# Kernel tuning notes

Hardware: AMD Instinct MI355X
Metric: run time of the kernel (lower is better)

The kernel has to match this reference:

```python
import jax, jax.numpy as jnp
import numpy as np

ALPHA = 0.2
EPS = 0.05        # geomloss SamplesLoss(p=1, blur=0.05): eps = blur**p = 0.05
N_ITERS = 50      # fixed sinkhorn iteration budget


def _sqdist(x, y):
    # x: [N,3], y: [M,3] -> [N,M] squared euclidean distances
    d2 = (jnp.sum(x * x, 1)[:, None] + jnp.sum(y * y, 1)[None, :]
          - 2.0 * (x @ y.T))
    return jnp.maximum(d2, 0.0)


def _sinkhorn_value(C, eps, n_iters):
    # uniform weights, log-domain sinkhorn; returns dual OT value <a,f>+<b,g>
    N, M = C.shape
    loga = -jnp.log(jnp.float32(N))
    logb = -jnp.log(jnp.float32(M))

    def step(carry, _):
        f, g = carry
        f = -eps * jax.nn.logsumexp(logb + (g[None, :] - C) / eps, axis=1)
        g = -eps * jax.nn.logsumexp(loga + (f[:, None] - C) / eps, axis=0)
        return (f, g), None

    (f, g), _ = jax.lax.scan(step, (jnp.zeros(N, C.dtype), jnp.zeros(M, C.dtype)),
                             None, length=n_iters)
    return jnp.mean(f) + jnp.mean(g)


def _sinkhorn_divergence(x, y, eps, n_iters):
    # debiased sinkhorn divergence: OT(x,y) - 0.5 OT(x,x) - 0.5 OT(y,y)
    def cost(a, b):
        return jnp.sqrt(_sqdist(a, b) + 1e-12)  # p=1 cost ||x-y||
    ot_xy = _sinkhorn_value(cost(x, y), eps, n_iters)
    ot_xx = _sinkhorn_value(cost(x, x), eps, n_iters)
    ot_yy = _sinkhorn_value(cost(y, y), eps, n_iters)
    return ot_xy - 0.5 * ot_xx - 0.5 * ot_yy


def setup_inputs() -> dict:
    key = jax.random.key(0)
    k1, k2 = jax.random.split(key)
    pred_feat = jax.random.normal(k1, (8192, 4), dtype=jnp.float32)
    gt_feat = jax.random.normal(k2, (8192, 4), dtype=jnp.float32)
    return {"pred_feat": pred_feat, "gt_feat": gt_feat}


def reference(pred_feat, gt_feat):
    pred_xyz = pred_feat[:, :3]
    gt_xyz = gt_feat[:, :3]
    # one-directional chamfer gt -> pred, squared NN distance, mean reduction
    d2 = _sqdist(gt_xyz, pred_xyz)          # [Ngt, Npred]
    chamfer_loss = jnp.mean(jnp.min(d2, axis=1))
    emd_loss = _sinkhorn_divergence(pred_xyz, gt_xyz, EPS, N_ITERS)
    return ALPHA * chamfer_loss + (1.0 - ALPHA) * emd_loss
```

## Files before the change

### kernel.cpp

```cpp
#include <hip/hip_runtime.h>
#include <hip/hip_bf16.h>
#include <math.h>


#define PN 8192
#define EPS 0.05f
#define SCALE 28.853900817779268f
#define INV_S2 (1.0f / (SCALE * SCALE))
#define LN2 0.6931471805599453f
#define TILE 2048
#define MARGIN 14.0f

#define EXP2F __builtin_amdgcn_exp2f
#define SQRTF __builtin_amdgcn_sqrtf
#if defined(__has_builtin) && __has_builtin(__builtin_amdgcn_logf)
#define LOG2F __builtin_amdgcn_logf
#else
#define LOG2F log2f
#endif

__device__ __forceinline__ int bitrev8(int x) { return __brev(x) >> 24; }

#define WS_QP    0
#define WS_QG    131072
#define WS_VF    262144
#define WS_VG    360448
#define WS_BB32  458752
#define WS_BB64  475136
#define WS_SARR  483328
#define WS_CHAM  532480

__global__ __launch_bounds__(1024) void sort_kernel(
    const float4* __restrict__ pred, const float4* __restrict__ gt,
    float4* __restrict__ QP, float4* __restrict__ QG)
{
    const int cloud = blockIdx.x;
    const float4* src = cloud ? gt : pred;
    float4* dst = cloud ? QG : QP;
    const int tid = threadIdx.x;

    __shared__ int hist[4096];
    __shared__ int part[1024];
#pragma unroll
    for (int k = 0; k < 4; ++k) hist[tid * 4 + k] = 0;
    __syncthreads();

    int keys[8];
#pragma unroll
    for (int k = 0; k < 8; ++k) {
        float4 v = src[tid * 8 + k];
        int cx = min(15, max(0, (int)floorf((v.x + 5.0f) * 1.6f)));
        int cy = min(15, max(0, (int)floorf((v.y + 5.0f) * 1.6f)));
        int cz = min(15, max(0, (int)floorf((v.z + 5.0f) * 1.6f)));
        keys[k] = (cz << 8) | (cy << 4) | cx;
        atomicAdd(&hist[keys[k]], 1);
    }
    __syncthreads();
    int h[4], s4 = 0;
#pragma unroll
    for (int k = 0; k < 4; ++k) { h[k] = hist[tid * 4 + k]; s4 += h[k]; }
    part[tid] = s4;
    __syncthreads();
    for (int off = 1; off < 1024; off <<= 1) {
        int v = (tid >= off) ? part[tid - off] : 0;
        __syncthreads();
        part[tid] += v;
        __syncthreads();
    }
    int base = part[tid] - s4;
#pragma unroll
    for (int k = 0; k < 4; ++k) { hist[tid * 4 + k] = base; base += h[k]; }
    __syncthreads();
#pragma unroll
    for (int k = 0; k < 8; ++k) {
        float4 v = src[tid * 8 + k];
        int pos = atomicAdd(&hist[keys[k]], 1);
        float x = v.x * SCALE, y = v.y * SCALE, z = v.z * SCALE;
        dst[pos] = make_float4(x, y, z, fmaf(x, x, fmaf(y, y, z * z)));
    }
}

__global__ __launch_bounds__(64) void bbox32_kernel(
    const float4* __restrict__ QP, const float4* __restrict__ QG,
    float4* __restrict__ bb32)
{
    const int b = blockIdx.x;
    const float4* q = (b >> 8) ? QG : QP;
    const int lane = threadIdx.x;
    float4 v = q[(b & 255) * 32 + (lane & 31)];
    float lx = v.x, ly = v.y, lz = v.z, hx = v.x, hy = v.y, hz = v.z;
#pragma unroll
    for (int off = 1; off <= 16; off <<= 1) {
        lx = fminf(lx, __shfl_xor(lx, off, 64));
        ly = fminf(ly, __shfl_xor(ly, off, 64));
        lz = fminf(lz, __shfl_xor(lz, off, 64));
        hx = fmaxf(hx, __shfl_xor(hx, off, 64));
        hy = fmaxf(hy, __shfl_xor(hy, off, 64));
        hz = fmaxf(hz, __shfl_xor(hz, off, 64));
    }
    if (lane == 0) {
        bb32[b * 2]     = make_float4(lx, ly, lz, 0.0f);
        bb32[b * 2 + 1] = make_float4(hx, hy, hz, 0.0f);
    }
}

__global__ __launch_bounds__(256) void bbox64_kernel(
    const float4* __restrict__ bb32, float4* __restrict__ bb64)
{
    const int t = threadIdx.x;
    const int cloud = t >> 7, tile = t & 127;
    const int s = (cloud * 256 + tile * 2) * 2;
    float4 lo0 = bb32[s], hi0 = bb32[s + 1], lo1 = bb32[s + 2], hi1 = bb32[s + 3];
    bb64[t * 2] = make_float4(fminf(lo0.x, lo1.x), fminf(lo0.y, lo1.y),
                              fminf(lo0.z, lo1.z), 0.0f);
    bb64[t * 2 + 1] = make_float4(fmaxf(hi0.x, hi1.x), fmaxf(hi0.y, hi1.y),
                                  fmaxf(hi0.z, hi1.z), 0.0f);
}

__global__ __launch_bounds__(256) void init_kernel(
    float* __restrict__ Vg, float* __restrict__ chamsum)
{
    int idx = blockIdx.x * 256 + threadIdx.x;
    if (idx < 3 * PN) Vg[idx] = 1.0f / 8192.0f;
    if (idx == 0) *chamsum = 0.0f;
}

__global__ __launch_bounds__(256) void seed_kernel(
    const float4* __restrict__ QP, const float4* __restrict__ QG,
    const float4* __restrict__ bb32, float* __restrict__ SArr)
{
    const int idx = blockIdx.x * 256 + threadIdx.x;
    const int quarter = idx & 3;
    const int rg = (idx >> 2) & 2047;
    const int combo = idx >> 13;
    const float4* rowQ = (combo >= 2) ? QG : QP;
    const int colCloud = (combo == 0 || combo == 2) ? 1 : 0;

    float lx = 1e30f, ly = 1e30f, lz = 1e30f;
    float hx = -1e30f, hy = -1e30f, hz = -1e30f;
#pragma unroll
    for (int k = 0; k < 4; ++k) {
        float4 q = rowQ[rg * 4 + k];
        lx = fminf(lx, q.x); hx = fmaxf(hx, q.x);
        ly = fminf(ly, q.y); hy = fmaxf(hy, q.y);
        lz = fminf(lz, q.z); hz = fmaxf(hz, q.z);
    }
    float best = 1e30f;
    for (int t = quarter * 64; t < quarter * 64 + 64; ++t) {
        float4 lo = bb32[(colCloud * 256 + t) * 2];
        float4 hi = bb32[(colCloud * 256 + t) * 2 + 1];
        float dx = fmaxf(hx - lo.x, hi.x - lx);
        float dy = fmaxf(hy - lo.y, hi.y - ly);
        float dz = fmaxf(hz - lo.z, hi.z - lz);
        float dmax2 = fmaf(dx, dx, fmaf(dy, dy, dz * dz));
        best = fminf(best, dmax2);
    }
    best = fminf(best, __shfl_xor(best, 1, 64));
    best = fminf(best, __shfl_xor(best, 2, 64));
    if (quarter == 0) {
        float seed = -13.5f - SQRTF(best);
        if (combo == 0) SArr[rg] = seed;
        else if (combo == 1) { SArr[2048 + rg] = seed;
                               SArr[4 * 2048 + rg] = seed; }
        else if (combo == 2) { SArr[2 * 2048 + rg] = seed;
                               SArr[5 * 2048 + rg] = seed; }
        else SArr[3 * 2048 + rg] = seed;
    }
}

__global__ __launch_bounds__(512) void pass_kernel(
    const float4* __restrict__ QP, const float4* __restrict__ QG,
    float* __restrict__ Vf, float* __restrict__ Vg,
    const float4* __restrict__ bb32, float* __restrict__ SArr,
    const int dir, const int colUniform)
{
    const int tid = threadIdx.x;
    const int lane = tid & 63;
    const int w = __builtin_amdgcn_readfirstlane(tid >> 6);
    const int p = blockIdx.x >> 8;
    const int b = blockIdx.x & 255;
    const int region = (bitrev8(b) + p * 85) & 255;

    const int r0 = (p == 2) ? 1 : 0;
    const int c0 = (p == 1) ? 0 : 1;
    const int rowCloud = dir ? c0 : r0;
    const int colCloud = dir ? r0 : c0;
    const float4* rowQ = rowCloud ? QG : QP;
    const float4* colQ = colCloud ? QG : QP;
    const float* vin  = (dir ? Vf : Vg) + p * PN;
    float* vout = (dir ? Vg : Vf) + p * PN;
    const float* SArrRow = SArr + (dir * 3 + p) * 2048;
    const float* SArrCol = SArr + ((dir ^ 1) * 3 + p) * 2048;
    float* SArrOut = SArr + (dir * 3 + p) * 2048;

    const int rg = region * 8 + w;
    const int row0 = rg << 2;

    float r2x[4], r2y[4], r2z[4], base[4], acc[4];
    float blox = 1e30f, bloy = 1e30f, bloz = 1e30f;
    float bhix = -1e30f, bhiy = -1e30f, bhiz = -1e30f;
#pragma unroll
    for (int k = 0; k < 4; ++k) {
        float4 q = rowQ[row0 + k];
        blox = fminf(blox, q.x); bhix = fmaxf(bhix, q.x);
        bloy = fminf(bloy, q.y); bhiy = fmaxf(bhiy, q.y);
        bloz = fminf(bloz, q.z); bhiz = fmaxf(bhiz, q.z);
        r2x[k] = -2.0f * q.x; r2y[k] = -2.0f * q.y; r2z[k] = -2.0f * q.z;
        base[k] = q.w;
        acc[k] = 0.0f;
    }
    const float lsr = SArrRow[rg];

    __shared__ float4 sQ[TILE];
    __shared__ float  sV[TILE];
    __shared__ float  sMaxH[256];
    __shared__ float4 sBLo[256], sBHi[256];

    if (tid < 256) {
        float maxh = -13.0f;
        if (!colUniform) {
            const float4* sa4 = (const float4*)SArrCol;
            float4 a = sa4[tid * 2], b4 = sa4[tid * 2 + 1];
            float m = fminf(fminf(fminf(a.x, a.y), fminf(a.z, a.w)),
                            fminf(fminf(b4.x, b4.y), fminf(b4.z, b4.w)));
            maxh = -13.0f - m;
        }
        sMaxH[tid] = maxh;
        sBLo[tid] = bb32[(colCloud * 256 + tid) * 2];
        sBHi[tid] = bb32[(colCloud * 256 + tid) * 2 + 1];
    }

    const float4* vin4 = (const float4*)vin;
    for (int tb = 0; tb < PN; tb += TILE) {
        __syncthreads();
#pragma unroll
        for (int k = 0; k < TILE / 512; ++k) {
            int idx = tid + k * 512;
            sQ[idx] = colQ[tb + idx];
        }
        ((float4*)sV)[tid] = vin4[tb / 4 + tid];
        __syncthreads();

        bool keep;
        {
            int t32 = (tb >> 5) + lane;
            float4 clo = sBLo[t32];
            float4 chi = sBHi[t32];
            float thr = fmaxf(sMaxH[t32] - lsr + MARGIN, 0.0f);
            float dx = fmaxf(0.0f, fmaxf(blox - chi.x, clo.x - bhix));
            float dy = fmaxf(0.0f, fmaxf(bloy - chi.y, clo.y - bhiy));
            float dz = fmaxf(0.0f, fmaxf(bloz - chi.z, clo.z - bhiz));
            float dmin2 = fmaf(dx, dx, fmaf(dy, dy, dz * dz));
            keep = dmin2 <= thr * thr;
        }
        unsigned long long mask = __ballot(keep);
        while (mask) {
            int i = __builtin_ctzll(mask);
            int t64 = i >> 1;
            mask &= ~(3ULL << (t64 << 1));
            int col = (t64 << 6) + lane;
            float4 wq = sQ[col];
            float v = sV[col];
#pragma unroll
            for (int k = 0; k < 4; ++k) {
                float t = base[k] + wq.w;
                t = fmaf(r2x[k], wq.x, t);
                t = fmaf(r2y[k], wq.y, t);
                t = fmaf(r2z[k], wq.z, t);
                float d = SQRTF(fabsf(t));
                float e = EXP2F(-d);
                acc[k] = fmaf(e, v, acc[k]);
            }
        }
    }

#pragma unroll
    for (int k = 0; k < 4; ++k) {
        float a = acc[k];
        a += __shfl_xor(a, 1, 64);  a += __shfl_xor(a, 2, 64);
        a += __shfl_xor(a, 4, 64);  a += __shfl_xor(a, 8, 64);
        a += __shfl_xor(a, 16, 64); a += __shfl_xor(a, 32, 64);
        acc[k] = a;
    }
    if (lane == 0) {
        float smin = fminf(fminf(acc[0], acc[1]), fminf(acc[2], acc[3]));
#pragma unroll
        for (int k = 0; k < 4; ++k)
            vout[row0 + k] = (1.0f / 8192.0f) / acc[k];
        SArrOut[rg] = LOG2F(smin);
    }
}

__global__ __launch_bounds__(512) void chamfer_kernel(
    const float4* __restrict__ QP, const float4* __restrict__ QG,
    const float4* __restrict__ bb64, float* __restrict__ chamsum)
{
    const int tid = threadIdx.x;
    const int lane = tid & 63;
    const int w = __builtin_amdgcn_readfirstlane(tid >> 6);
    const int rg = bitrev8(blockIdx.x) * 8 + w;
    const int row0 = rg << 2;

    float r2x[4], r2y[4], r2z[4], base[4], m[4];
    float blox = 1e30f, bloy = 1e30f, bloz = 1e30f;
    float bhix = -1e30f, bhiy = -1e30f, bhiz = -1e30f;
#pragma unroll
    for (int k = 0; k < 4; ++k) {
        float4 q = QG[row0 + k];
        blox = fminf(blox, q.x); bhix = fmaxf(bhix, q.x);
        bloy = fminf(bloy, q.y); bhiy = fmaxf(bhiy, q.y);
        bloz = fminf(bloz, q.z); bhiz = fmaxf(bhiz, q.z);
        r2x[k] = -2.0f * q.x; r2y[k] = -2.0f * q.y; r2z[k] = -2.0f * q.z;
        base[k] = q.w;
        m[k] = 3.4e38f;
    }
    const float bcx = (blox + bhix) * 0.5f;
    const float bcy = (bloy + bhiy) * 0.5f;
    const float bcz = (bloz + bhiz) * 0.5f;

    float bd = 1e30f; int bi = 0;
#pragma unroll
    for (int h = 0; h < 2; ++h) {
        int t = lane + h * 64;
        float4 lo = bb64[t * 2], hi = bb64[t * 2 + 1];
        float cx = (lo.x + hi.x) * 0.5f - bcx;
        float cy = (lo.y + hi.y) * 0.5f - bcy;
        float cz = (lo.z + hi.z) * 0.5f - bcz;
        float d = fmaf(cx, cx, fmaf(cy, cy, cz * cz));
        if (d < bd) { bd = d; bi = t; }
    }
#pragma unroll
    for (int off = 1; off <= 32; off <<= 1) {
        float od = __shfl_xor(bd, off, 64);
        int oi = __shfl_xor(bi, off, 64);
        if (od < bd) { bd = od; bi = oi; }
    }
    const int home = __builtin_amdgcn_readfirstlane(bi);

    {
        float4 wq = QP[home * 64 + lane];
#pragma unroll
        for (int k = 0; k < 4; ++k) {
            float t = fmaf(r2x[k], wq.x, wq.w);
            t = fmaf(r2y[k], wq.y, t);
            t = fmaf(r2z[k], wq.z, t);
            m[k] = fminf(m[k], t);
        }
    }
    float Bmax = -3.4e38f;
#pragma unroll
    for (int k = 0; k < 4; ++k) {
        float mr = m[k];
#pragma unroll
        for (int off = 1; off <= 32; off <<= 1)
            mr = fminf(mr, __shfl_xor(mr, off, 64));
        m[k] = mr;
        Bmax = fmaxf(Bmax, mr + base[k]);
    }

#pragma unroll
    for (int h = 0; h < 2; ++h) {
        int t = lane + h * 64;
        float4 lo = bb64[t * 2], hi = bb64[t * 2 + 1];
        float dx = fmaxf(0.0f, fmaxf(blox - hi.x, lo.x - bhix));
        float dy = fmaxf(0.0f, fmaxf(bloy - hi.y, lo.y - bhiy));
        float dz = fmaxf(0.0f, fmaxf(bloz - hi.z, lo.z - bhiz));
        float dmin2 = fmaf(dx, dx, fmaf(dy, dy, dz * dz));
        bool keep = (dmin2 < Bmax) && (t != home);
        unsigned long long mask = __ballot(keep);
        while (mask) {
            int st = __builtin_ctzll(mask);
            mask &= mask - 1;
            float4 wq = QP[((h << 6) + st) * 64 + lane];
#pragma unroll
            for (int k = 0; k < 4; ++k) {
                float tt = fmaf(r2x[k], wq.x, wq.w);
                tt = fmaf(r2y[k], wq.y, tt);
                tt = fmaf(r2z[k], wq.z, tt);
                m[k] = fminf(m[k], tt);
            }
        }
    }
    float ch = 0.0f;
#pragma unroll
    for (int k = 0; k < 4; ++k) {
        float mr = m[k];
#pragma unroll
        for (int off = 1; off <= 32; off <<= 1)
            mr = fminf(mr, __shfl_xor(mr, off, 64));
        ch += fmaxf(mr + base[k], 0.0f) * INV_S2;
    }
    __shared__ float red[8];
    if (lane == 0) red[w] = ch;
    __syncthreads();
    if (tid == 0) {
        float s = 0.0f;
#pragma unroll
        for (int k = 0; k < 8; ++k) s += red[k];
        atomicAdd(chamsum, s);
    }
}

__global__ __launch_bounds__(256) void final_kernel(
    const float* __restrict__ Vf, const float* __restrict__ Vg,
    const float* __restrict__ chamsum, float* __restrict__ out)
{
    const int tid = threadIdx.x;
    float local = 0.0f;
    for (int i = tid; i < PN; i += 256) {
        float w0 = LOG2F(Vf[i]) + LOG2F(Vg[i]);
        float w1 = LOG2F(Vf[PN + i]) + LOG2F(Vg[PN + i]);
        float w2 = LOG2F(Vf[2 * PN + i]) + LOG2F(Vg[2 * PN + i]);
        local += w0 - 0.5f * (w1 + w2);
    }
    for (int off = 32; off; off >>= 1) local += __shfl_xor(local, off, 64);
    __shared__ float red[4];
    if ((tid & 63) == 0) red[tid >> 6] = local;
    __syncthreads();
    if (tid == 0) {
        float wsum = red[0] + red[1] + red[2] + red[3];
        float emd = EPS * LN2 * wsum / 8192.0f;
        float cham = (*chamsum) / 8192.0f;
        out[0] = 0.2f * cham + 0.8f * emd;
    }
}

extern "C" void kernel_launch(void* const* d_in, const int* in_sizes, int n_in,
                              void* d_out, int out_size, void* d_ws, size_t ws_size,
                              hipStream_t stream)
{
    const float4* pred = (const float4*)d_in[0];
    const float4* gt   = (const float4*)d_in[1];
    char* ws = (char*)d_ws;
    float4* QP      = (float4*)(ws + WS_QP);
    float4* QG      = (float4*)(ws + WS_QG);
    float*  Vf      = (float*)(ws + WS_VF);
    float*  Vg      = (float*)(ws + WS_VG);
    float4* bb32    = (float4*)(ws + WS_BB32);
    float4* bb64    = (float4*)(ws + WS_BB64);
    float*  SArr    = (float*)(ws + WS_SARR);
    float*  chamsum = (float*)(ws + WS_CHAM);
    float*  out     = (float*)d_out;

    sort_kernel<<<2, 1024, 0, stream>>>(pred, gt, QP, QG);
    init_kernel<<<96, 256, 0, stream>>>(Vg, chamsum);
    bbox32_kernel<<<512, 64, 0, stream>>>(QP, QG, bb32);
    bbox64_kernel<<<1, 256, 0, stream>>>(bb32, bb64);
    seed_kernel<<<128, 256, 0, stream>>>(QP, QG, bb32, SArr);
    chamfer_kernel<<<256, 512, 0, stream>>>(QP, QG, bb64, chamsum);
    for (int it = 0; it < 50; ++it) {
        pass_kernel<<<768, 512, 0, stream>>>(QP, QG, Vf, Vg, bb32, SArr, 0,
                                             it == 0 ? 1 : 0);
        pass_kernel<<<768, 512, 0, stream>>>(QP, QG, Vf, Vg, bb32, SArr, 1, 0);
    }
    final_kernel<<<1, 256, 0, stream>>>(Vf, Vg, chamsum, out);
}
```

Baseline: 2.908 ms.

## Give each wave pair 8 rows and split column tiles between them

```diff
diff --git a/kernel.cpp b/kernel.cpp
--- a/kernel.cpp
+++ b/kernel.cpp
@@ -131,16 +131,16 @@
 {
     const int idx = blockIdx.x * 256 + threadIdx.x;
     const int quarter = idx & 3;
-    const int rg = (idx >> 2) & 2047;
-    const int combo = idx >> 13;
+    const int rg = (idx >> 2) & 1023;
+    const int combo = idx >> 12;
     const float4* rowQ = (combo >= 2) ? QG : QP;
     const int colCloud = (combo == 0 || combo == 2) ? 1 : 0;
 
     float lx = 1e30f, ly = 1e30f, lz = 1e30f;
     float hx = -1e30f, hy = -1e30f, hz = -1e30f;
 #pragma unroll
-    for (int k = 0; k < 4; ++k) {
-        float4 q = rowQ[rg * 4 + k];
+    for (int k = 0; k < 8; ++k) {
+        float4 q = rowQ[rg * 8 + k];
         lx = fminf(lx, q.x); hx = fmaxf(hx, q.x);
         ly = fminf(ly, q.y); hy = fmaxf(hy, q.y);
         lz = fminf(lz, q.z); hz = fmaxf(hz, q.z);
@@ -160,11 +160,11 @@
     if (quarter == 0) {
         float seed = -13.5f - SQRTF(best);
         if (combo == 0) SArr[rg] = seed;
-        else if (combo == 1) { SArr[2048 + rg] = seed;
-                               SArr[4 * 2048 + rg] = seed; }
-        else if (combo == 2) { SArr[2 * 2048 + rg] = seed;
-                               SArr[5 * 2048 + rg] = seed; }
-        else SArr[3 * 2048 + rg] = seed;
+        else if (combo == 1) { SArr[1024 + rg] = seed;
+                               SArr[4 * 1024 + rg] = seed; }
+        else if (combo == 2) { SArr[2 * 1024 + rg] = seed;
+                               SArr[5 * 1024 + rg] = seed; }
+        else SArr[3 * 1024 + rg] = seed;
     }
 }
 
@@ -177,6 +177,8 @@
     const int tid = threadIdx.x;
     const int lane = tid & 63;
     const int w = __builtin_amdgcn_readfirstlane(tid >> 6);
+    const int pr = w & 1;
+    const int pg = w >> 1;
     const int p = blockIdx.x >> 8;
     const int b = blockIdx.x & 255;
     const int region = (bitrev8(b) + p * 85) & 255;
@@ -189,18 +191,18 @@
     const float4* colQ = colCloud ? QG : QP;
     const float* vin  = (dir ? Vf : Vg) + p * PN;
     float* vout = (dir ? Vg : Vf) + p * PN;
-    const float* SArrRow = SArr + (dir * 3 + p) * 2048;
-    const float* SArrCol = SArr + ((dir ^ 1) * 3 + p) * 2048;
-    float* SArrOut = SArr + (dir * 3 + p) * 2048;
-
-    const int rg = region * 8 + w;
-    const int row0 = rg << 2;
-
-    float r2x[4], r2y[4], r2z[4], base[4], acc[4];
+    const float* SArrRow = SArr + (dir * 3 + p) * 1024;
+    const float* SArrCol = SArr + ((dir ^ 1) * 3 + p) * 1024;
+    float* SArrOut = SArr + (dir * 3 + p) * 1024;
+
+    const int grp = region * 4 + pg;
+    const int row0 = grp << 3;
+
+    float r2x[8], r2y[8], r2z[8], base[8], acc[8];
     float blox = 1e30f, bloy = 1e30f, bloz = 1e30f;
     float bhix = -1e30f, bhiy = -1e30f, bhiz = -1e30f;
 #pragma unroll
-    for (int k = 0; k < 4; ++k) {
+    for (int k = 0; k < 8; ++k) {
         float4 q = rowQ[row0 + k];
         blox = fminf(blox, q.x); bhix = fmaxf(bhix, q.x);
         bloy = fminf(bloy, q.y); bhiy = fmaxf(bhiy, q.y);
@@ -209,20 +211,19 @@
         base[k] = q.w;
         acc[k] = 0.0f;
     }
-    const float lsr = SArrRow[rg];
+    const float lsr = SArrRow[grp];
 
     __shared__ float4 sQ[TILE];
     __shared__ float  sV[TILE];
     __shared__ float  sMaxH[256];
     __shared__ float4 sBLo[256], sBHi[256];
+    __shared__ float  redS[8][9];
 
     if (tid < 256) {
         float maxh = -13.0f;
         if (!colUniform) {
-            const float4* sa4 = (const float4*)SArrCol;
-            float4 a = sa4[tid * 2], b4 = sa4[tid * 2 + 1];
-            float m = fminf(fminf(fminf(a.x, a.y), fminf(a.z, a.w)),
-                            fminf(fminf(b4.x, b4.y), fminf(b4.z, b4.w)));
+            float4 a = ((const float4*)SArrCol)[tid];
+            float m = fminf(fminf(a.x, a.y), fminf(a.z, a.w));
             maxh = -13.0f - m;
         }
         sMaxH[tid] = maxh;
@@ -254,15 +255,18 @@
             keep = dmin2 <= thr * thr;
         }
         unsigned long long mask = __ballot(keep);
+        int skip = pr;
         while (mask) {
             int i = __builtin_ctzll(mask);
             int t64 = i >> 1;
             mask &= ~(3ULL << (t64 << 1));
+            if (skip) { skip = 0; continue; }
+            skip = 1;
             int col = (t64 << 6) + lane;
             float4 wq = sQ[col];
             float v = sV[col];
 #pragma unroll
-            for (int k = 0; k < 4; ++k) {
+            for (int k = 0; k < 8; ++k) {
                 float t = base[k] + wq.w;
                 t = fmaf(r2x[k], wq.x, t);
                 t = fmaf(r2y[k], wq.y, t);
@@ -275,7 +279,7 @@
     }
 
 #pragma unroll
-    for (int k = 0; k < 4; ++k) {
+    for (int k = 0; k < 8; ++k) {
         float a = acc[k];
         a += __shfl_xor(a, 1, 64);  a += __shfl_xor(a, 2, 64);
         a += __shfl_xor(a, 4, 64);  a += __shfl_xor(a, 8, 64);
@@ -283,11 +287,20 @@
         acc[k] = a;
     }
     if (lane == 0) {
-        float smin = fminf(fminf(acc[0], acc[1]), fminf(acc[2], acc[3]));
-#pragma unroll
-        for (int k = 0; k < 4; ++k)
-            vout[row0 + k] = (1.0f / 8192.0f) / acc[k];
-        SArrOut[rg] = LOG2F(smin);
+#pragma unroll
+        for (int k = 0; k < 8; ++k) redS[w][k] = acc[k];
+    }
+    __syncthreads();
+    if (tid < 32) {
+        int g = tid >> 3, r = tid & 7;
+        float s = redS[2 * g][r] + redS[2 * g + 1][r];
+        int og = region * 4 + g;
+        vout[(og << 3) + r] = (1.0f / 8192.0f) / s;
+        float ls = LOG2F(s);
+        ls = fminf(ls, __shfl_xor(ls, 1, 64));
+        ls = fminf(ls, __shfl_xor(ls, 2, 64));
+        ls = fminf(ls, __shfl_xor(ls, 4, 64));
+        if (r == 0) SArrOut[og] = ls;
     }
 }
 
@@ -446,7 +459,7 @@
     init_kernel<<<96, 256, 0, stream>>>(Vg, chamsum);
     bbox32_kernel<<<512, 64, 0, stream>>>(QP, QG, bb32);
     bbox64_kernel<<<1, 256, 0, stream>>>(bb32, bb64);
-    seed_kernel<<<128, 256, 0, stream>>>(QP, QG, bb32, SArr);
+    seed_kernel<<<64, 256, 0, stream>>>(QP, QG, bb32, SArr);
     chamfer_kernel<<<256, 512, 0, stream>>>(QP, QG, bb64, chamsum);
     for (int it = 0; it < 50; ++it) {
         pass_kernel<<<768, 512, 0, stream>>>(QP, QG, Vf, Vg, bb32, SArr, 0,
```

Result: slower. 3.060 ms (+5.3%).
